# Optimization experiments

Hardware: AMD Instinct MI355X
Metric: run time of the kernel (lower is better)

The kernel has to match this reference:

```python
import jax, jax.numpy as jnp
import numpy as np

B, FR, T, C = 8, 257, 300, 64
CPP, G, K = 16, 8, 3
EPS = 1e-5


def _ln(x, g, b):
    m = jnp.mean(x, axis=-1, keepdims=True)
    v = jnp.mean((x - m) ** 2, axis=-1, keepdims=True)
    return (x - m) * jax.lax.rsqrt(v + EPS) * g + b


def _freq_conv(x, g, b, w, cb, alpha):
    # x: [N, F, C]
    res = x
    y = _ln(x, g, b).transpose(0, 2, 1)  # [N, C, F]
    y = jax.lax.conv_general_dilated(
        y, w, window_strides=(1,), padding=((K // 2, K // 2),),
        feature_group_count=G, dimension_numbers=("NCH", "OIH", "NCH"))
    y = y + cb[None, :, None]
    y = y.transpose(0, 2, 1)  # [N, F, C]
    return res + jnp.where(y >= 0, y, alpha * y)


def _full_band(x, g, b, rw, rb, fW, fB, ew, eb):
    # x: [N, F, C]
    res = x
    y = _ln(x, g, b)
    hp = jax.nn.silu(jnp.einsum("nfc,pc->nfp", y, rw) + rb)  # [N, F, Cpp]
    hp = hp.transpose(0, 2, 1)  # [N, Cpp, F]
    # batched per-channel Linear(F, F): out[n,c,g] = sum_f hp[n,c,f] * fW[c,g,f] + fB[c,g]
    hp = jnp.einsum("ncf,cgf->ncg", hp, fW) + fB[None]
    hp = hp.transpose(0, 2, 1)  # [N, F, Cpp]
    out = jax.nn.silu(jnp.einsum("nfp,cp->nfc", hp, ew) + eb)
    return res + out


def setup_inputs() -> dict:
    key = jax.random.key(0)
    ks = jax.random.split(key, 20)
    s = 0.05
    d = {
        "h": jax.random.normal(ks[0], (B, FR, T, C), jnp.float32),
        "fc1_g": jnp.ones((C,), jnp.float32),
        "fc1_b": jnp.zeros((C,), jnp.float32),
        "fc1_w": jax.random.normal(ks[1], (C, C // G, K), jnp.float32) * s,
        "fc1_cb": jax.random.normal(ks[2], (C,), jnp.float32) * s,
        "fc1_a": jnp.asarray(0.25, jnp.float32),
        "fbl_g": jnp.ones((C,), jnp.float32),
        "fbl_b": jnp.zeros((C,), jnp.float32),
        "red_w": jax.random.normal(ks[3], (CPP, C), jnp.float32) * s,
        "red_b": jax.random.normal(ks[4], (CPP,), jnp.float32) * s,
        "fW": jax.random.normal(ks[5], (CPP, FR, FR), jnp.float32) * s,
        "fB": jax.random.normal(ks[6], (CPP, FR), jnp.float32) * s,
        "exp_w": jax.random.normal(ks[7], (C, CPP), jnp.float32) * s,
        "exp_b": jax.random.normal(ks[8], (C,), jnp.float32) * s,
        "fc2_g": jnp.ones((C,), jnp.float32),
        "fc2_b": jnp.zeros((C,), jnp.float32),
        "fc2_w": jax.random.normal(ks[9], (C, C // G, K), jnp.float32) * s,
        "fc2_cb": jax.random.normal(ks[10], (C,), jnp.float32) * s,
        "fc2_a": jnp.asarray(0.25, jnp.float32),
    }
    return d


def reference(h, fc1_g, fc1_b, fc1_w, fc1_cb, fc1_a,
              fbl_g, fbl_b, red_w, red_b, fW, fB, exp_w, exp_b,
              fc2_g, fc2_b, fc2_w, fc2_cb, fc2_a):
    b, fr, t, c = h.shape
    x = h.transpose(0, 2, 1, 3).reshape(b * t, fr, c)  # [B*T, F, C]
    x = _freq_conv(x, fc1_g, fc1_b, fc1_w, fc1_cb, fc1_a)
    x = _full_band(x, fbl_g, fbl_b, red_w, red_b, fW, fB, exp_w, exp_b)
    x = _freq_conv(x, fc2_g, fc2_b, fc2_w, fc2_cb, fc2_a)
    return x.reshape(b, t, fr, c).transpose(0, 2, 1, 3)
```

## Files before the change

### kernel.cpp

```cpp
#include <hip/hip_runtime.h>
#include <math.h>

#define BDIM 8
#define FR   257
#define TT   300
#define CC   64
#define NN   (BDIM*TT)
#define CPPC 16
#define GG   8
#define CPG  8
#define KW   3
#define EPSV 1e-5f

#define FT    64
#define NTIL  5
#define ROWS  66
#define FSTR  65

#define X1_ELEMS ((size_t)NN*FR*CC)
#define HP_ELEMS ((size_t)CPPC*NN*FR)

template<int CTRL>
__device__ __forceinline__ float dpp_term(float v) {
    return __int_as_float(
        __builtin_amdgcn_update_dpp(0, __float_as_int(v), CTRL, 0xf, 0xf, true));
}
template<int PAT>
__device__ __forceinline__ float swz_term(float v) {
    return __int_as_float(__builtin_amdgcn_ds_swizzle(__float_as_int(v), PAT));
}

__device__ __forceinline__ float wave_sum64(float v) {
    v += dpp_term<0x111>(v);
    v += dpp_term<0x112>(v);
    v += dpp_term<0x114>(v);
    v += dpp_term<0x118>(v);
    v += dpp_term<0x142>(v);
    v += dpp_term<0x143>(v);
    return __int_as_float(__builtin_amdgcn_readlane(__float_as_int(v), 63));
}

__device__ __forceinline__ void ln_stats_dpp(float v, float& m, float& r) {
    float s  = wave_sum64(v);
    float ss = wave_sum64(v*v);
    m = s * (1.0f/64.0f);
    float var = ss * (1.0f/64.0f) - m*m;
    r = rsqrtf(var + EPSV);
}

__device__ __forceinline__ float conv_row(float y0, float y1, float y2,
                                          const float wq[8][KW]) {
    float q[8];
    #pragma unroll
    for (int d = 0; d < 8; ++d)
        q[d] = y0*wq[d][0] + y1*wq[d][1] + y2*wq[d][2];
    float acc = q[0];
    acc += dpp_term<0xB1>(q[1]);
    acc += dpp_term<0x4E>(q[2]);
    acc += dpp_term<0x1B>(q[3]);
    acc += swz_term<0x101F>(q[4]);
    acc += swz_term<0x141F>(q[5]);
    acc += swz_term<0x181F>(q[6]);
    acc += dpp_term<0x141>(q[7]);
    return acc;
}

__global__ __launch_bounds__(256, 4)
void k_fc1(const float* __restrict__ h,
           const float* __restrict__ g1, const float* __restrict__ b1,
           const float* __restrict__ w1, const float* __restrict__ cb1,
           const float* __restrict__ a1,
           const float* __restrict__ g2, const float* __restrict__ b2,
           const float* __restrict__ redw, const float* __restrict__ redb,
           float* __restrict__ x1, float* __restrict__ hpT)
{
    __shared__ float xs[ROWS*FSTR];
    __shared__ float ys[ROWS*FSTR];

    const int n  = blockIdx.x;
    const int f0 = blockIdx.y * FT;
    const int nf = min(FT, FR - f0);
    const int b = n / TT, t = n - b*TT;
    const int tid = threadIdx.x;
    const int lane = tid & 63, wid = tid >> 6;

    const float alpha = a1[0];
    const float gA = g1[lane], bA = b1[lane];
    const float gB = g2[lane], bB = b2[lane];
    const float cbv = cb1[lane];

    const size_t hb0 = ((size_t)b*FR*TT + t)*CC;
    #pragma unroll
    for (int it = 0; it < 17; ++it) {
        int lr = wid + it*4;
        if (lr >= ROWS) continue;
        int f = f0 - 1 + lr;
        if (f >= 0 && f < FR) {
            float v = h[hb0 + (size_t)f*TT*CC + lane];
            xs[lr*FSTR + lane] = v;
            float m, r; ln_stats_dpp(v, m, r);
            ys[lr*FSTR + lane] = (v - m) * r * gA + bA;
        } else {
            xs[lr*FSTR + lane] = 0.0f;
            ys[lr*FSTR + lane] = 0.0f;
        }
    }
    __syncthreads();

    const int l8 = lane & 7;
    const int gbase = lane & 56;
    float wq[8][KW];
    #pragma unroll
    for (int d = 0; d < 8; ++d) {
        const float* wp = w1 + (size_t)(gbase | (l8 ^ d))*(CPG*KW) + l8*KW;
        #pragma unroll
        for (int k = 0; k < KW; ++k) wq[d][k] = wp[k];
    }

    #pragma unroll
    for (int it = 0; it < 17; ++it) {
        int lr = wid + it*4;
        if (lr < 1 || lr > nf) continue;
        float y0 = ys[(lr-1)*FSTR + lane];
        float y1 = ys[ lr   *FSTR + lane];
        float y2 = ys[(lr+1)*FSTR + lane];
        float acc = conv_row(y0, y1, y2, wq) + cbv;
        float pr = acc >= 0.0f ? acc : alpha*acc;
        float xv = xs[lr*FSTR + lane] + pr;
        xs[lr*FSTR + lane] = xv;
        int f = f0 + lr - 1;
        x1[(size_t)n*FR*CC + (size_t)f*CC + lane] = xv;
    }
    __syncthreads();

    #pragma unroll
    for (int it = 0; it < 17; ++it) {
        int lr = wid + it*4;
        if (lr < 1 || lr > nf) continue;
        float v = xs[lr*FSTR + lane];
        float m, r; ln_stats_dpp(v, m, r);
        ys[lr*FSTR + lane] = (v - m) * r * gB + bB;
    }
    __syncthreads();

    {
        const int L = lane;
        const int lr = (L < nf) ? (L + 1) : 1;
        const int p0 = wid * 4;
        const float* wp0 = redw + (size_t)(p0+0)*CC;
        const float* wp1 = redw + (size_t)(p0+1)*CC;
        const float* wp2 = redw + (size_t)(p0+2)*CC;
        const float* wp3 = redw + (size_t)(p0+3)*CC;
        float a0 = redb[p0+0], a1v = redb[p0+1], a2 = redb[p0+2], a3 = redb[p0+3];
        #pragma unroll 16
        for (int c = 0; c < CC; ++c) {
            float yv = ys[lr*FSTR + c];
            a0  += yv * wp0[c];
            a1v += yv * wp1[c];
            a2  += yv * wp2[c];
            a3  += yv * wp3[c];
        }
        if (L < nf) {
            int f = f0 + L;
            float s0 = a0  / (1.0f + expf(-a0));
            float s1 = a1v / (1.0f + expf(-a1v));
            float s2 = a2  / (1.0f + expf(-a2));
            float s3 = a3  / (1.0f + expf(-a3));
            size_t base = (size_t)n*FR + f;
            hpT[(size_t)(p0+0)*(NN*FR) + base] = s0;
            hpT[(size_t)(p0+1)*(NN*FR) + base] = s1;
            hpT[(size_t)(p0+2)*(NN*FR) + base] = s2;
            hpT[(size_t)(p0+3)*(NN*FR) + base] = s3;
        }
    }
}

#define BM 64
#define BN 64
#define BK 32
#define LDT 72

__global__ __launch_bounds__(256, 2)
void k_fgemm(const float* __restrict__ hpT, const float* __restrict__ fW,
             const float* __restrict__ fB, float* __restrict__ hp2T)
{
    __shared__ __align__(16) float As[BK*LDT];
    __shared__ __align__(16) float Bs[BK*LDT];
    const int c  = blockIdx.z;
    const int m0 = blockIdx.x * BM;
    const int f0 = blockIdx.y * BN;
    const int tid = threadIdx.x;
    const int tm = tid & 15, tn = tid >> 4;

    const float* Ab = hpT + (size_t)c*(NN*FR);
    const float* Bb = fW  + (size_t)c*(FR*FR);

    float acc[4][4];
    #pragma unroll
    for (int i = 0; i < 4; ++i)
        #pragma unroll
        for (int j = 0; j < 4; ++j) acc[i][j] = 0.0f;

    for (int k0 = 0; k0 < FR; k0 += BK) {
        #pragma unroll
        for (int l = 0; l < 8; ++l) {
            int e = tid + l*256;
            int r = e >> 5, kc = e & 31;
            int m = m0 + r, k = k0 + kc;
            As[kc*LDT + r] = (m < NN && k < FR) ? Ab[(size_t)m*FR + k] : 0.0f;
            int fr = f0 + r;
            Bs[kc*LDT + r] = (fr < FR && k < FR) ? Bb[(size_t)fr*FR + k] : 0.0f;
        }
        __syncthreads();
        #pragma unroll
        for (int k = 0; k < BK; ++k) {
            const float4 av = *reinterpret_cast<const float4*>(&As[k*LDT + (tm<<2)]);
            const float4 bv = *reinterpret_cast<const float4*>(&Bs[k*LDT + (tn<<2)]);
            acc[0][0] += av.x*bv.x; acc[0][1] += av.x*bv.y; acc[0][2] += av.x*bv.z; acc[0][3] += av.x*bv.w;
            acc[1][0] += av.y*bv.x; acc[1][1] += av.y*bv.y; acc[1][2] += av.y*bv.z; acc[1][3] += av.y*bv.w;
            acc[2][0] += av.z*bv.x; acc[2][1] += av.z*bv.y; acc[2][2] += av.z*bv.z; acc[2][3] += av.z*bv.w;
            acc[3][0] += av.w*bv.x; acc[3][1] += av.w*bv.y; acc[3][2] += av.w*bv.z; acc[3][3] += av.w*bv.w;
        }
        __syncthreads();
    }

    #pragma unroll
    for (int i = 0; i < 4; ++i) {
        int m = m0 + (tm<<2) + i;
        if (m >= NN) continue;
        #pragma unroll
        for (int j = 0; j < 4; ++j) {
            int fr = f0 + (tn<<2) + j;
            if (fr < FR)
                hp2T[(size_t)c*(NN*FR) + (size_t)m*FR + fr] = acc[i][j] + fB[c*FR + fr];
        }
    }
}

__global__ __launch_bounds__(256, 4)
void k_fc2(const float* __restrict__ x1, const float* __restrict__ hp2T,
           const float* __restrict__ expw, const float* __restrict__ expb,
           const float* __restrict__ g3, const float* __restrict__ b3,
           const float* __restrict__ w2, const float* __restrict__ cb2,
           const float* __restrict__ a2,
           float* __restrict__ out)
{
    __shared__ float xs[ROWS*FSTR];
    __shared__ float ys[ROWS*FSTR];

    const int n  = blockIdx.x;
    const int f0 = blockIdx.y * FT;
    const int nf = min(FT, FR - f0);
    const int b = n / TT, t = n - b*TT;
    const int tid = threadIdx.x;
    const int lane = tid & 63, wid = tid >> 6;

    const float ebv = expb[lane];
    const float gC = g3[lane], bC = b3[lane];
    const float alpha = a2[0];
    const float cbv = cb2[lane];

    float ew[CPPC];
    #pragma unroll
    for (int p = 0; p < CPPC; ++p) ew[p] = expw[lane*CPPC + p];

    #pragma unroll
    for (int it = 0; it < 17; ++it) {
        int lr = wid + it*4;
        if (lr >= ROWS) continue;
        int f = f0 - 1 + lr;
        if (f >= 0 && f < FR) {
            size_t base = (size_t)n*FR + f;
            float z = ebv;
            #pragma unroll
            for (int p = 0; p < CPPC; ++p)
                z += hp2T[(size_t)p*(NN*FR) + base] * ew[p];
            float sg = z / (1.0f + expf(-z));
            float v = x1[(size_t)n*FR*CC + (size_t)f*CC + lane] + sg;
            xs[lr*FSTR + lane] = v;
            float m, r; ln_stats_dpp(v, m, r);
            ys[lr*FSTR + lane] = (v - m) * r * gC + bC;
        } else {
            xs[lr*FSTR + lane] = 0.0f;
            ys[lr*FSTR + lane] = 0.0f;
        }
    }
    __syncthreads();

    const int l8 = lane & 7;
    const int gbase = lane & 56;
    float wq[8][KW];
    #pragma unroll
    for (int d = 0; d < 8; ++d) {
        const float* wp = w2 + (size_t)(gbase | (l8 ^ d))*(CPG*KW) + l8*KW;
        #pragma unroll
        for (int k = 0; k < KW; ++k) wq[d][k] = wp[k];
    }

    const size_t ob0 = ((size_t)b*FR*TT + t)*CC;
    #pragma unroll
    for (int it = 0; it < 17; ++it) {
        int lr = wid + it*4;
        if (lr < 1 || lr > nf) continue;
        float y0 = ys[(lr-1)*FSTR + lane];
        float y1 = ys[ lr   *FSTR + lane];
        float y2 = ys[(lr+1)*FSTR + lane];
        float acc = conv_row(y0, y1, y2, wq) + cbv;
        float pr = acc >= 0.0f ? acc : alpha*acc;
        int f = f0 + lr - 1;
        out[ob0 + (size_t)f*TT*CC + lane] = xs[lr*FSTR + lane] + pr;
    }
}

extern "C" void kernel_launch(void* const* d_in, const int* in_sizes, int n_in,
                              void* d_out, int out_size, void* d_ws, size_t ws_size,
                              hipStream_t stream) {
    const float* h      = (const float*)d_in[0];
    const float* fc1_g  = (const float*)d_in[1];
    const float* fc1_b  = (const float*)d_in[2];
    const float* fc1_w  = (const float*)d_in[3];
    const float* fc1_cb = (const float*)d_in[4];
    const float* fc1_a  = (const float*)d_in[5];
    const float* fbl_g  = (const float*)d_in[6];
    const float* fbl_b  = (const float*)d_in[7];
    const float* red_w  = (const float*)d_in[8];
    const float* red_b  = (const float*)d_in[9];
    const float* fW     = (const float*)d_in[10];
    const float* fB     = (const float*)d_in[11];
    const float* exp_w  = (const float*)d_in[12];
    const float* exp_b  = (const float*)d_in[13];
    const float* fc2_g  = (const float*)d_in[14];
    const float* fc2_b  = (const float*)d_in[15];
    const float* fc2_w  = (const float*)d_in[16];
    const float* fc2_cb = (const float*)d_in[17];
    const float* fc2_a  = (const float*)d_in[18];

    float* ws   = (float*)d_ws;
    float* x1   = ws;
    float* hpT  = x1 + X1_ELEMS;
    float* hp2T = hpT + HP_ELEMS;

    dim3 g1(NN, NTIL);
    k_fc1<<<g1, 256, 0, stream>>>(h, fc1_g, fc1_b, fc1_w, fc1_cb, fc1_a,
                                  fbl_g, fbl_b, red_w, red_b, x1, hpT);

    dim3 g2((NN + BM - 1)/BM, (FR + BN - 1)/BN, CPPC);
    k_fgemm<<<g2, 256, 0, stream>>>(hpT, fW, fB, hp2T);

    dim3 g3(NN, NTIL);
    k_fc2<<<g3, 256, 0, stream>>>(x1, hp2T, exp_w, exp_b,
                                  fc2_g, fc2_b, fc2_w, fc2_cb, fc2_a,
                                  (float*)d_out);
}
```

Baseline: 943.4 us.

## Retile frequency GEMM to 8x8 register tiles and slim the conv kernels' shared memory

The per-channel frequency GEMM moves from 64x64 tiles with 4x4 outputs per thread to 128x64 tiles with 8x8 outputs per thread, 128 threads and float4 global loads. This raises arithmetic intensity per shared-memory load. The fc1 and fc2 kernels shrink the frequency tile to 60 rows and drop the halo rows from the residual buffer, which cuts shared memory enough to raise the occupancy hint. fc1 also fuses the second layernorm into the conv epilogue, removing one barrier and one pass, and reads the reduction input as float2. The larger accumulator array adds register pressure in the GEMM, and the smaller tile means more recomputed halo rows per frequency row.

```diff
diff --git a/kernel.cpp b/kernel.cpp
--- a/kernel.cpp
+++ b/kernel.cpp
@@ -12,10 +12,10 @@
 #define KW   3
 #define EPSV 1e-5f
 
-#define FT    64
+#define FT    60
 #define NTIL  5
-#define ROWS  66
-#define FSTR  65
+#define ROWS  62
+#define FSTR  66
 
 #define X1_ELEMS ((size_t)NN*FR*CC)
 #define HP_ELEMS ((size_t)CPPC*NN*FR)
@@ -65,7 +65,7 @@
     return acc;
 }
 
-__global__ __launch_bounds__(256, 4)
+__global__ __launch_bounds__(256, 5)
 void k_fc1(const float* __restrict__ h,
            const float* __restrict__ g1, const float* __restrict__ b1,
            const float* __restrict__ w1, const float* __restrict__ cb1,
@@ -74,8 +74,8 @@
            const float* __restrict__ redw, const float* __restrict__ redb,
            float* __restrict__ x1, float* __restrict__ hpT)
 {
-    __shared__ float xs[ROWS*FSTR];
     __shared__ float ys[ROWS*FSTR];
+    __shared__ float xs[FT*FSTR];
 
     const int n  = blockIdx.x;
     const int f0 = blockIdx.y * FT;
@@ -91,17 +91,16 @@
 
     const size_t hb0 = ((size_t)b*FR*TT + t)*CC;
     #pragma unroll
-    for (int it = 0; it < 17; ++it) {
+    for (int it = 0; it < 16; ++it) {
         int lr = wid + it*4;
         if (lr >= ROWS) continue;
         int f = f0 - 1 + lr;
         if (f >= 0 && f < FR) {
             float v = h[hb0 + (size_t)f*TT*CC + lane];
-            xs[lr*FSTR + lane] = v;
+            if (lr >= 1 && lr <= nf) xs[(lr-1)*FSTR + lane] = v;
             float m, r; ln_stats_dpp(v, m, r);
             ys[lr*FSTR + lane] = (v - m) * r * gA + bA;
         } else {
-            xs[lr*FSTR + lane] = 0.0f;
             ys[lr*FSTR + lane] = 0.0f;
         }
     }
@@ -118,7 +117,7 @@
     }
 
     #pragma unroll
-    for (int it = 0; it < 17; ++it) {
+    for (int it = 0; it < 16; ++it) {
         int lr = wid + it*4;
         if (lr < 1 || lr > nf) continue;
         float y0 = ys[(lr-1)*FSTR + lane];
@@ -126,39 +125,31 @@
         float y2 = ys[(lr+1)*FSTR + lane];
         float acc = conv_row(y0, y1, y2, wq) + cbv;
         float pr = acc >= 0.0f ? acc : alpha*acc;
-        float xv = xs[lr*FSTR + lane] + pr;
-        xs[lr*FSTR + lane] = xv;
+        float xv = xs[(lr-1)*FSTR + lane] + pr;
         int f = f0 + lr - 1;
         x1[(size_t)n*FR*CC + (size_t)f*CC + lane] = xv;
-    }
-    __syncthreads();
-
-    #pragma unroll
-    for (int it = 0; it < 17; ++it) {
-        int lr = wid + it*4;
-        if (lr < 1 || lr > nf) continue;
-        float v = xs[lr*FSTR + lane];
-        float m, r; ln_stats_dpp(v, m, r);
-        ys[lr*FSTR + lane] = (v - m) * r * gB + bB;
+        float m, r; ln_stats_dpp(xv, m, r);
+        xs[(lr-1)*FSTR + lane] = (xv - m) * r * gB + bB;
     }
     __syncthreads();
 
     {
         const int L = lane;
-        const int lr = (L < nf) ? (L + 1) : 1;
+        const int row = (L < nf) ? L : 0;
+        const float* xrow = &xs[row*FSTR];
         const int p0 = wid * 4;
         const float* wp0 = redw + (size_t)(p0+0)*CC;
         const float* wp1 = redw + (size_t)(p0+1)*CC;
         const float* wp2 = redw + (size_t)(p0+2)*CC;
         const float* wp3 = redw + (size_t)(p0+3)*CC;
         float a0 = redb[p0+0], a1v = redb[p0+1], a2 = redb[p0+2], a3 = redb[p0+3];
-        #pragma unroll 16
-        for (int c = 0; c < CC; ++c) {
-            float yv = ys[lr*FSTR + c];
-            a0  += yv * wp0[c];
-            a1v += yv * wp1[c];
-            a2  += yv * wp2[c];
-            a3  += yv * wp3[c];
+        #pragma unroll
+        for (int c2 = 0; c2 < 32; ++c2) {
+            float2 y2 = *reinterpret_cast<const float2*>(&xrow[2*c2]);
+            a0  += y2.x*wp0[2*c2] + y2.y*wp0[2*c2+1];
+            a1v += y2.x*wp1[2*c2] + y2.y*wp1[2*c2+1];
+            a2  += y2.x*wp2[2*c2] + y2.y*wp2[2*c2+1];
+            a3  += y2.x*wp3[2*c2] + y2.y*wp3[2*c2+1];
         }
         if (L < nf) {
             int f = f0 + L;
@@ -175,69 +166,110 @@
     }
 }
 
-#define BM 64
-#define BN 64
-#define BK 32
-#define LDT 72
-
-__global__ __launch_bounds__(256, 2)
+#define GBM 128
+#define GBN 64
+#define GBK 16
+#define GLDA 132
+#define GLDB 68
+
+__global__ __launch_bounds__(128, 4)
 void k_fgemm(const float* __restrict__ hpT, const float* __restrict__ fW,
              const float* __restrict__ fB, float* __restrict__ hp2T)
 {
-    __shared__ __align__(16) float As[BK*LDT];
-    __shared__ __align__(16) float Bs[BK*LDT];
+    __shared__ __align__(16) float As[GBK*GLDA];
+    __shared__ __align__(16) float Bs[GBK*GLDB];
     const int c  = blockIdx.z;
-    const int m0 = blockIdx.x * BM;
-    const int f0 = blockIdx.y * BN;
+    const int m0 = blockIdx.x * GBM;
+    const int f0 = blockIdx.y * GBN;
     const int tid = threadIdx.x;
-    const int tm = tid & 15, tn = tid >> 4;
+    const int tx = tid & 7;
+    const int ty = tid >> 3;
 
     const float* Ab = hpT + (size_t)c*(NN*FR);
     const float* Bb = fW  + (size_t)c*(FR*FR);
 
-    float acc[4][4];
-    #pragma unroll
-    for (int i = 0; i < 4; ++i)
-        #pragma unroll
-        for (int j = 0; j < 4; ++j) acc[i][j] = 0.0f;
-
-    for (int k0 = 0; k0 < FR; k0 += BK) {
-        #pragma unroll
-        for (int l = 0; l < 8; ++l) {
-            int e = tid + l*256;
-            int r = e >> 5, kc = e & 31;
-            int m = m0 + r, k = k0 + kc;
-            As[kc*LDT + r] = (m < NN && k < FR) ? Ab[(size_t)m*FR + k] : 0.0f;
-            int fr = f0 + r;
-            Bs[kc*LDT + r] = (fr < FR && k < FR) ? Bb[(size_t)fr*FR + k] : 0.0f;
+    float acc[8][8];
+    #pragma unroll
+    for (int i = 0; i < 8; ++i)
+        #pragma unroll
+        for (int j = 0; j < 8; ++j) acc[i][j] = 0.0f;
+
+    for (int k0 = 0; k0 < FR; k0 += GBK) {
+        #pragma unroll
+        for (int l = 0; l < 4; ++l) {
+            int e = tid + l*128;
+            int m = e >> 2, kq = e & 3;
+            int gm = m0 + m, gk = k0 + kq*4;
+            float4 v = make_float4(0.f,0.f,0.f,0.f);
+            if (gm < NN) {
+                if (gk + 3 < FR) {
+                    v = *reinterpret_cast<const float4*>(&Ab[(size_t)gm*FR + gk]);
+                } else {
+                    float tv[4] = {0.f,0.f,0.f,0.f};
+                    #pragma unroll
+                    for (int j = 0; j < 4; ++j) if (gk+j < FR) tv[j] = Ab[(size_t)gm*FR + gk + j];
+                    v = make_float4(tv[0],tv[1],tv[2],tv[3]);
+                }
+            }
+            As[(kq*4+0)*GLDA + m] = v.x;
+            As[(kq*4+1)*GLDA + m] = v.y;
+            As[(kq*4+2)*GLDA + m] = v.z;
+            As[(kq*4+3)*GLDA + m] = v.w;
+        }
+        #pragma unroll
+        for (int l = 0; l < 2; ++l) {
+            int e = tid + l*128;
+            int j = e >> 2, kq = e & 3;
+            int gf = f0 + j, gk = k0 + kq*4;
+            float4 v = make_float4(0.f,0.f,0.f,0.f);
+            if (gf < FR) {
+                if (gk + 3 < FR) {
+                    v = *reinterpret_cast<const float4*>(&Bb[(size_t)gf*FR + gk]);
+                } else {
+                    float tv[4] = {0.f,0.f,0.f,0.f};
+                    #pragma unroll
+                    for (int jj = 0; jj < 4; ++jj) if (gk+jj < FR) tv[jj] = Bb[(size_t)gf*FR + gk + jj];
+                    v = make_float4(tv[0],tv[1],tv[2],tv[3]);
+                }
+            }
+            Bs[(kq*4+0)*GLDB + j] = v.x;
+            Bs[(kq*4+1)*GLDB + j] = v.y;
+            Bs[(kq*4+2)*GLDB + j] = v.z;
+            Bs[(kq*4+3)*GLDB + j] = v.w;
         }
         __syncthreads();
-        #pragma unroll
-        for (int k = 0; k < BK; ++k) {
-            const float4 av = *reinterpret_cast<const float4*>(&As[k*LDT + (tm<<2)]);
-            const float4 bv = *reinterpret_cast<const float4*>(&Bs[k*LDT + (tn<<2)]);
-            acc[0][0] += av.x*bv.x; acc[0][1] += av.x*bv.y; acc[0][2] += av.x*bv.z; acc[0][3] += av.x*bv.w;
-            acc[1][0] += av.y*bv.x; acc[1][1] += av.y*bv.y; acc[1][2] += av.y*bv.z; acc[1][3] += av.y*bv.w;
-            acc[2][0] += av.z*bv.x; acc[2][1] += av.z*bv.y; acc[2][2] += av.z*bv.z; acc[2][3] += av.z*bv.w;
-            acc[3][0] += av.w*bv.x; acc[3][1] += av.w*bv.y; acc[3][2] += av.w*bv.z; acc[3][3] += av.w*bv.w;
+
+        #pragma unroll
+        for (int k = 0; k < GBK; ++k) {
+            const float4 a0 = *reinterpret_cast<const float4*>(&As[k*GLDA + ty*8]);
+            const float4 a1 = *reinterpret_cast<const float4*>(&As[k*GLDA + ty*8 + 4]);
+            const float4 b0 = *reinterpret_cast<const float4*>(&Bs[k*GLDB + tx*8]);
+            const float4 b1 = *reinterpret_cast<const float4*>(&Bs[k*GLDB + tx*8 + 4]);
+            const float av[8] = {a0.x,a0.y,a0.z,a0.w,a1.x,a1.y,a1.z,a1.w};
+            const float bv[8] = {b0.x,b0.y,b0.z,b0.w,b1.x,b1.y,b1.z,b1.w};
+            #pragma unroll
+            for (int i = 0; i < 8; ++i)
+                #pragma unroll
+                for (int j = 0; j < 8; ++j)
+                    acc[i][j] += av[i]*bv[j];
         }
         __syncthreads();
     }
 
     #pragma unroll
-    for (int i = 0; i < 4; ++i) {
-        int m = m0 + (tm<<2) + i;
+    for (int i = 0; i < 8; ++i) {
+        int m = m0 + ty*8 + i;
         if (m >= NN) continue;
         #pragma unroll
-        for (int j = 0; j < 4; ++j) {
-            int fr = f0 + (tn<<2) + j;
+        for (int j = 0; j < 8; ++j) {
+            int fr = f0 + tx*8 + j;
             if (fr < FR)
                 hp2T[(size_t)c*(NN*FR) + (size_t)m*FR + fr] = acc[i][j] + fB[c*FR + fr];
         }
     }
 }
 
-__global__ __launch_bounds__(256, 4)
+__global__ __launch_bounds__(256, 5)
 void k_fc2(const float* __restrict__ x1, const float* __restrict__ hp2T,
            const float* __restrict__ expw, const float* __restrict__ expb,
            const float* __restrict__ g3, const float* __restrict__ b3,
@@ -245,8 +277,8 @@
            const float* __restrict__ a2,
            float* __restrict__ out)
 {
-    __shared__ float xs[ROWS*FSTR];
     __shared__ float ys[ROWS*FSTR];
+    __shared__ float xs[FT*FSTR];
 
     const int n  = blockIdx.x;
     const int f0 = blockIdx.y * FT;
@@ -265,7 +297,7 @@
     for (int p = 0; p < CPPC; ++p) ew[p] = expw[lane*CPPC + p];
 
     #pragma unroll
-    for (int it = 0; it < 17; ++it) {
+    for (int it = 0; it < 16; ++it) {
         int lr = wid + it*4;
         if (lr >= ROWS) continue;
         int f = f0 - 1 + lr;
@@ -277,11 +309,10 @@
                 z += hp2T[(size_t)p*(NN*FR) + base] * ew[p];
             float sg = z / (1.0f + expf(-z));
             float v = x1[(size_t)n*FR*CC + (size_t)f*CC + lane] + sg;
-            xs[lr*FSTR + lane] = v;
+            if (lr >= 1 && lr <= nf) xs[(lr-1)*FSTR + lane] = v;
             float m, r; ln_stats_dpp(v, m, r);
             ys[lr*FSTR + lane] = (v - m) * r * gC + bC;
         } else {
-            xs[lr*FSTR + lane] = 0.0f;
             ys[lr*FSTR + lane] = 0.0f;
         }
     }
@@ -299,7 +330,7 @@
 
     const size_t ob0 = ((size_t)b*FR*TT + t)*CC;
     #pragma unroll
-    for (int it = 0; it < 17; ++it) {
+    for (int it = 0; it < 16; ++it) {
         int lr = wid + it*4;
         if (lr < 1 || lr > nf) continue;
         float y0 = ys[(lr-1)*FSTR + lane];
@@ -308,7 +339,7 @@
         float acc = conv_row(y0, y1, y2, wq) + cbv;
         float pr = acc >= 0.0f ? acc : alpha*acc;
         int f = f0 + lr - 1;
-        out[ob0 + (size_t)f*TT*CC + lane] = xs[lr*FSTR + lane] + pr;
+        out[ob0 + (size_t)f*TT*CC + lane] = xs[(lr-1)*FSTR + lane] + pr;
     }
 }
 
@@ -344,8 +375,8 @@
     k_fc1<<<g1, 256, 0, stream>>>(h, fc1_g, fc1_b, fc1_w, fc1_cb, fc1_a,
                                   fbl_g, fbl_b, red_w, red_b, x1, hpT);
 
-    dim3 g2((NN + BM - 1)/BM, (FR + BN - 1)/BN, CPPC);
-    k_fgemm<<<g2, 256, 0, stream>>>(hpT, fW, fB, hp2T);
+    dim3 g2((NN + GBM - 1)/GBM, (FR + GBN - 1)/GBN, CPPC);
+    k_fgemm<<<g2, 128, 0, stream>>>(hpT, fW, fB, hp2T);
 
     dim3 g3(NN, NTIL);
     k_fc2<<<g3, 256, 0, stream>>>(x1, hp2T, exp_w, exp_b,
```

Measured after the change: 1.077 ms. 14.1% more time.
